# Performance work log

Measured on AMD Instinct MI355X. Metric: run time of the kernel, lower is better.

Reference implementation:

```python
import jax, jax.numpy as jnp
import numpy as np

NUM_HEADS = 16
ROPE_BASE = 2048.0


def _rope_tables(seq_len, head_dim, dtype):
    inv_freq = 1.0 / (ROPE_BASE ** (jnp.arange(0, head_dim, 2, dtype=jnp.float32) / head_dim))
    t = jnp.arange(seq_len, dtype=jnp.float32)
    freqs = jnp.einsum('i,j->ij', t, inv_freq)          # [N, D/2]
    emb = jnp.concatenate([freqs, freqs], axis=-1)       # [N, D]
    return jnp.cos(emb).astype(dtype), jnp.sin(emb).astype(dtype)


def _rotate_half(x):
    x1, x2 = jnp.split(x, 2, axis=-1)
    return jnp.concatenate([-x2, x1], axis=-1)


def setup_inputs() -> dict:
    key = jax.random.key(0)
    k1, k2, k3, k4 = jax.random.split(key, 4)
    B, N, C = 2, 2048, 1024
    x = jax.random.normal(k1, (B, N, C), dtype=jnp.float32)
    w_qkv = jax.random.normal(k2, (3 * C, C), dtype=jnp.float32) * (C ** -0.5)
    w_proj = jax.random.normal(k3, (C, C), dtype=jnp.float32) * (C ** -0.5)
    b_proj = jnp.zeros((C,), dtype=jnp.float32)
    key_padding_mask = jax.random.randint(k4, (B, N), 0, 2, dtype=jnp.int32)
    return {"x": x, "w_qkv": w_qkv, "w_proj": w_proj, "b_proj": b_proj,
            "key_padding_mask": key_padding_mask}


def reference(x, w_qkv, w_proj, b_proj, key_padding_mask):
    B, N, C = x.shape
    H = NUM_HEADS
    D = C // H
    scale = D ** -0.5

    qkv = x @ w_qkv.T                                    # [B, N, 3C]
    q, k, v = jnp.split(qkv, 3, axis=-1)
    # [B, N, C] -> [B, H, N, D]
    q = q.reshape(B, N, H, D).transpose(0, 2, 1, 3)
    k = k.reshape(B, N, H, D).transpose(0, 2, 1, 3)
    v = v.reshape(B, N, H, D).transpose(0, 2, 1, 3)

    cos, sin = _rope_tables(N, D, x.dtype)               # [N, D]
    q = q * cos + _rotate_half(q) * sin
    k = k * cos + _rotate_half(k) * sin

    attn = jnp.einsum('bhqd,bhkd->bhqk', q, k) * scale   # [B, H, N, N]
    mask = (key_padding_mask == 0)[:, None, None, :]     # [B, 1, 1, N]
    attn = jnp.where(mask, jnp.asarray(-1e9, attn.dtype), attn)
    attn = jax.nn.softmax(attn, axis=-1)

    out = jnp.einsum('bhqk,bhkd->bhqd', attn, v)         # [B, H, N, D]
    out = out.transpose(0, 2, 1, 3).reshape(B, N, C)
    return out @ w_proj.T + b_proj
```

## Files before the change

### kernel.cpp

```cpp
#include <hip/hip_runtime.h>


typedef __attribute__((ext_vector_type(8))) short          s16x8;
typedef __attribute__((ext_vector_type(8))) unsigned short u16x8;
typedef __attribute__((ext_vector_type(4))) unsigned short u16x4;
typedef __attribute__((ext_vector_type(4))) float          f32x4;
typedef __attribute__((ext_vector_type(16))) float         f32x16;
typedef __attribute__((ext_vector_type(4))) unsigned int   u32x4;

#define MFMA_BF16(a, b, c) __builtin_amdgcn_mfma_f32_16x16x32_bf16((a), (b), (c), 0, 0, 0)
#define MFMA32_BF16(a, b, c) __builtin_amdgcn_mfma_f32_32x32x16_bf16((a), (b), (c), 0, 0, 0)

#define GLD_TO_LDS(gp, lp) __builtin_amdgcn_global_load_lds(                  \
    (const __attribute__((address_space(1))) void*)(gp),                      \
    (__attribute__((address_space(3))) void*)(lp), 16, 0, 0)

__device__ __forceinline__ unsigned short f2bf(float f) {
    union { float f; unsigned int u; } v; v.f = f;
    unsigned int u = v.u;
    unsigned int r = u + 0x7FFFu + ((u >> 16) & 1u);
    return (unsigned short)(r >> 16);
}
__device__ __forceinline__ float bf2f(unsigned short h) {
    union { unsigned int u; float f; } v; v.u = ((unsigned int)h) << 16;
    return v.f;
}
__device__ __forceinline__ f32x16 zero16() {
    f32x16 z;
#pragma unroll
    for (int i = 0; i < 16; i++) z[i] = 0.f;
    return z;
}
__device__ __forceinline__ unsigned int pkbf(float a, float b) {
    return __builtin_amdgcn_perm(__builtin_bit_cast(unsigned int, b),
                                 __builtin_bit_cast(unsigned int, a), 0x07060302u);
}
__device__ __forceinline__ int perm16(int p) {
    return (p & 3) + 8 * ((p >> 2) & 1) + 4 * (p >> 3);
}

__global__ __launch_bounds__(256) void prep(const float* __restrict__ x,
                                            const float* __restrict__ wqkv,
                                            const float* __restrict__ wproj,
                                            const int* __restrict__ m,
                                            unsigned short* __restrict__ xb,
                                            unsigned short* __restrict__ wqkvb,
                                            unsigned short* __restrict__ wprojb,
                                            unsigned short* __restrict__ mb) {
    int blk = blockIdx.x, tid = threadIdx.x;
    if (blk < 4096) {
        const float* src; unsigned short* dst; int i;
        if (blk < 2048)      { src = x;     dst = xb;     i = blk * 256 + tid; }
        else if (blk < 3584) { src = wqkv;  dst = wqkvb;  i = (blk - 2048) * 256 + tid; }
        else                 { src = wproj; dst = wprojb; i = (blk - 3584) * 256 + tid; }
        f32x4 v0 = ((const f32x4*)src)[i * 2];
        f32x4 v1 = ((const f32x4*)src)[i * 2 + 1];
        u16x8 o;
        o[0] = f2bf(v0[0]); o[1] = f2bf(v0[1]); o[2] = f2bf(v0[2]); o[3] = f2bf(v0[3]);
        o[4] = f2bf(v1[0]); o[5] = f2bf(v1[1]); o[6] = f2bf(v1[2]); o[7] = f2bf(v1[3]);
        ((u16x8*)dst)[i] = o;
    } else {
        int i = (blk - 4096) * 256 + tid;
        int src = (i & ~15) | perm16(i & 15);
        mb[i] = (m[src] == 0) ? (unsigned short)0 : (unsigned short)0x3F80;
    }
}

__global__ __launch_bounds__(256) void gemm_bt(const unsigned short* __restrict__ A,
                                               const unsigned short* __restrict__ B,
                                               unsigned short* __restrict__ C,
                                               int M, int N, int K) {
    __shared__ unsigned short Al[128][64];
    __shared__ unsigned short Bl[128][64];
    const int tid  = threadIdx.x;
    const int lane = tid & 63;
    const int qd   = lane >> 4;
    const int cc   = lane & 15;
    const int wave = tid >> 6;
    const int wr   = wave >> 1, wc = wave & 1;
    const int nbx  = N >> 7;
    const int nwg  = gridDim.x;
    int d = blockIdx.x;
    int s = (nwg % 8 == 0) ? (d % 8) * (nwg / 8) + d / 8 : d;
    const int m0   = (s / nbx) * 128, n0 = (s % nbx) * 128;
    unsigned short* Alf = &Al[0][0];
    unsigned short* Blf = &Bl[0][0];

    f32x4 acc[4][4];
#pragma unroll
    for (int i = 0; i < 4; i++)
#pragma unroll
        for (int j = 0; j < 4; j++) acc[i][j] = (f32x4){0.f, 0.f, 0.f, 0.f};

    for (int k0 = 0; k0 < K; k0 += 64) {
#pragma unroll
        for (int t = 0; t < 4; t++) {
            int idx = t * 256 + tid;
            int row = idx >> 3, sg = (idx & 7) ^ (row & 7);
            GLD_TO_LDS(A + (size_t)(m0 + row) * K + k0 + sg * 8, Alf + idx * 8);
            GLD_TO_LDS(B + (size_t)(n0 + row) * K + k0 + sg * 8, Blf + idx * 8);
        }
        __syncthreads();
#pragma unroll
        for (int ks = 0; ks < 64; ks += 32) {
            const int s4 = ks >> 3;
            s16x8 af[4], bf[4];
#pragma unroll
            for (int i = 0; i < 4; i++) {
                int r = wr * 64 + i * 16 + cc;
                af[i] = *(const s16x8*)&Al[r][((s4 + qd) ^ (r & 7)) * 8];
            }
#pragma unroll
            for (int j = 0; j < 4; j++) {
                int r = wc * 64 + j * 16 + cc;
                bf[j] = *(const s16x8*)&Bl[r][((s4 + qd) ^ (r & 7)) * 8];
            }
#pragma unroll
            for (int i = 0; i < 4; i++)
#pragma unroll
                for (int j = 0; j < 4; j++)
                    acc[i][j] = MFMA_BF16(af[i], bf[j], acc[i][j]);
        }
        __syncthreads();
    }
#pragma unroll
    for (int i = 0; i < 4; i++)
#pragma unroll
        for (int j = 0; j < 4; j++)
#pragma unroll
            for (int r = 0; r < 4; r++) {
                int row = m0 + wr * 64 + i * 16 + qd * 4 + r;
                int col = n0 + wc * 64 + j * 16 + cc;
                C[(size_t)row * N + col] = f2bf(acc[i][j][r]);
            }
}

__global__ __launch_bounds__(256) void rope_scatter(const unsigned short* __restrict__ qkv,
                                                    const int* __restrict__ msk,
                                                    unsigned short* __restrict__ Kg,
                                                    unsigned short* __restrict__ Vt) {
    const int N = 2048, H = 16, D = 64, C3 = 3072;
    __shared__ unsigned short vl[64][65];
    const int nt = blockIdx.x, h = blockIdx.y, b = blockIdx.z;
    const int n0 = nt * 64;
    const int tid = threadIdx.x;
    const size_t bh = (size_t)b * H + h;
#pragma unroll
    for (int it = 0; it < 2; it++) {
        int idx = tid + it * 256;
        int row = idx >> 3, seg = idx & 7;
        int d0 = seg * 8;
        int n = n0 + row;
        size_t rb = ((size_t)b * N + n) * C3;
        int keep = msk[(size_t)b * N + n];
        u16x8 kv = *(const u16x8*)&qkv[rb + 1024 + h * 64 + d0];
        u16x8 kp = *(const u16x8*)&qkv[rb + 1024 + h * 64 + (d0 ^ 32)];
        u16x8 vv = *(const u16x8*)&qkv[rb + 2048 + h * 64 + d0];
        u16x8 ko;
        float sgn = (d0 < 32) ? -1.0f : 1.0f;
#pragma unroll
        for (int j = 0; j < 8; j++) {
            int jj = (d0 & 31) + j;
            float th = (float)n * exp2f(-0.34375f * (float)jj);
            float cth = __cosf(th), sth = __sinf(th);
            ko[j] = f2bf(bf2f(kv[j]) * cth + sgn * bf2f(kp[j]) * sth);
            vl[row][d0 + j] = keep ? vv[j] : (unsigned short)0;
        }
        *(u16x8*)&Kg[(bh * N + n) * D + d0] = ko;
    }
    __syncthreads();
#pragma unroll
    for (int it = 0; it < 2; it++) {
        int idx = tid + it * 256;
        int drow = idx >> 3, nseg = idx & 7;
        u16x8 ov;
#pragma unroll
        for (int j = 0; j < 8; j++) {
            int cpos = nseg * 8 + j;
            int srcl = (cpos & ~15) | perm16(cpos & 15);
            ov[j] = vl[srcl][drow];
        }
        *(u16x8*)&Vt[(bh * D + drow) * N + n0 + nseg * 8] = ov;
    }
}

__global__ __launch_bounds__(256, 2) void flash_attn(const unsigned short* __restrict__ qkvp,
                                                     const unsigned short* __restrict__ Kg,
                                                     const unsigned short* __restrict__ Vt,
                                                     const unsigned short* __restrict__ mb,
                                                     unsigned short* __restrict__ Og) {
    const int N = 2048, H = 16, D = 64;
    const float SCL = 0.18033688f;
    __shared__ unsigned short ldsbuf[4 * 64 * 64];
    unsigned short (*Kl0)[64] = (unsigned short(*)[64])(ldsbuf);
    unsigned short (*Kl1)[64] = (unsigned short(*)[64])(ldsbuf + 4096);
    unsigned short (*Vl0)[64] = (unsigned short(*)[64])(ldsbuf + 8192);
    unsigned short (*Vl1)[64] = (unsigned short(*)[64])(ldsbuf + 12288);
    const int tid  = threadIdx.x;
    const int lane = tid & 63;
    const int wave = tid >> 6;
    const int qhalf = wave & 1;
    const int khalf = wave >> 1;
    const int c    = lane & 31;
    const int hi   = lane >> 5;
    int dd = blockIdx.x;
    int sw = (dd & 7) * 64 + (dd >> 3);
    const int qt = sw & 15, h = (sw >> 4) & 15, b = sw >> 8;
    const int q0 = qt * 128;
    const size_t bh = (size_t)b * H + h;

    s16x8 qf[2][4];
    {
        s16x8 qraw[2][4];
#pragma unroll
        for (int qs = 0; qs < 2; qs++) {
            const unsigned short* Qb =
                qkvp + ((size_t)b * N + q0 + qhalf * 64 + qs * 32 + c) * 3072 + h * 64;
#pragma unroll
            for (int kd = 0; kd < 4; kd++)
                qraw[qs][kd] = *(const s16x8*)(Qb + kd * 16 + hi * 8);
        }
#pragma unroll
        for (int qs = 0; qs < 2; qs++) {
            float nn = (float)(q0 + qhalf * 64 + qs * 32 + c);
#pragma unroll
            for (int kd = 0; kd < 4; kd++) {
                float sgn = (kd < 2) ? -1.0f : 1.0f;
#pragma unroll
                for (int j = 0; j < 8; j++) {
                    int jj = (kd & 1) * 16 + hi * 8 + j;
                    float th = nn * exp2f(-0.34375f * (float)jj);
                    float cth = __cosf(th), sth = __sinf(th);
                    float v = bf2f((unsigned short)qraw[qs][kd][j]);
                    float p = bf2f((unsigned short)qraw[qs][kd ^ 2][j]);
                    qf[qs][kd][j] = (short)f2bf((v * cth + sgn * p * sth) * SCL);
                }
            }
        }
    }

    f32x16 o[2][2], lacc[2];
#pragma unroll
    for (int qs = 0; qs < 2; qs++) {
        o[qs][0] = zero16(); o[qs][1] = zero16(); lacc[qs] = zero16();
    }

    const unsigned short* Kbase = Kg + bh * N * D;
    const unsigned short* Vbase = Vt + bh * D * N;
    const unsigned short* mbase = mb + (size_t)b * N;
    const int row_s = tid >> 3, sg_s = (tid & 7) ^ ((tid >> 3) & 7);
    const int row_s2 = (tid + 256) >> 3, sg_s2 = (tid & 7) ^ (((tid + 256) >> 3) & 7);

    auto issue = [&](int k0, unsigned short* Kb, unsigned short* Vb) {
        GLD_TO_LDS(Kbase + (size_t)(k0 + row_s) * D + sg_s * 8,   Kb + tid * 8);
        GLD_TO_LDS(Vbase + (size_t)row_s * N + k0 + sg_s * 8,     Vb + tid * 8);
        GLD_TO_LDS(Kbase + (size_t)(k0 + row_s2) * D + sg_s2 * 8, Kb + (tid + 256) * 8);
        GLD_TO_LDS(Vbase + (size_t)row_s2 * N + k0 + sg_s2 * 8,   Vb + (tid + 256) * 8);
    };

    auto compute = [&](int k0, const unsigned short (*Kb)[64], const unsigned short (*Vb)[64]) {
        auto packkg = [&](const f32x16& sstv, s16x8* pa) {
            float p[16];
#pragma unroll
            for (int r = 0; r < 16; r++) p[r] = __builtin_amdgcn_exp2f(sstv[r]);
#pragma unroll
            for (int half = 0; half < 2; half++) {
                int bs = half * 8;
                u32x4 w = { pkbf(p[bs + 0], p[bs + 1]), pkbf(p[bs + 2], p[bs + 3]),
                            pkbf(p[bs + 4], p[bs + 5]), pkbf(p[bs + 6], p[bs + 7]) };
                pa[half] = __builtin_bit_cast(s16x8, w);
            }
        };

        int kr = khalf * 32 + c;
        s16x8 kf[4];
#pragma unroll
        for (int kd = 0; kd < 4; kd++)
            kf[kd] = *(const s16x8*)&Kb[kr][((kd * 2 + hi) ^ (kr & 7)) * 8];
        f32x16 sst0 = zero16(), sst1 = zero16();
        __builtin_amdgcn_s_setprio(1);
#pragma unroll
        for (int kd = 0; kd < 4; kd++) {
            sst0 = MFMA32_BF16(kf[kd], qf[0][kd], sst0);
            sst1 = MFMA32_BF16(kf[kd], qf[1][kd], sst1);
        }
        __builtin_amdgcn_s_setprio(0);
        s16x8 pa[2][2];
        packkg(sst0, pa[0]);
        packkg(sst1, pa[1]);

#pragma unroll
        for (int ksl = 0; ksl < 2; ksl++) {
            int ks = khalf * 2 + ksl;
            s16x8 mfr = *(const s16x8*)&mbase[k0 + ks * 16 + hi * 8];
            int vr0 = c, vr1 = 32 + c;
            s16x8 vf0 = *(const s16x8*)&Vb[vr0][((ks * 2 + hi) ^ (vr0 & 7)) * 8];
            s16x8 vf1 = *(const s16x8*)&Vb[vr1][((ks * 2 + hi) ^ (vr1 & 7)) * 8];
            __builtin_amdgcn_s_setprio(1);
#pragma unroll
            for (int qs = 0; qs < 2; qs++) {
                lacc[qs]  = MFMA32_BF16(pa[qs][ksl], mfr, lacc[qs]);
                o[qs][0]  = MFMA32_BF16(pa[qs][ksl], vf0, o[qs][0]);
                o[qs][1]  = MFMA32_BF16(pa[qs][ksl], vf1, o[qs][1]);
            }
            __builtin_amdgcn_s_setprio(0);
        }
    };

    issue(0, &Kl0[0][0], &Vl0[0][0]);
    __syncthreads();
    for (int it = 0; it < 32; it += 2) {
        int k0 = it * 64;
        if (it + 1 < 32) issue(k0 + 64, &Kl1[0][0], &Vl1[0][0]);
        compute(k0, Kl0, Vl0);
        __syncthreads();
        if (it + 2 < 32) issue(k0 + 128, &Kl0[0][0], &Vl0[0][0]);
        compute(k0 + 64, Kl1, Vl1);
        __syncthreads();
    }

    float* red = (float*)ldsbuf;
#pragma unroll
    for (int qs = 0; qs < 2; qs++) {
        __syncthreads();
        if (khalf == 1) {
            float* dst = red + qhalf * 3136 + lane * 49;
#pragma unroll
            for (int r = 0; r < 16; r++) {
                dst[r] = o[qs][0][r]; dst[16 + r] = o[qs][1][r]; dst[32 + r] = lacc[qs][r];
            }
        }
        __syncthreads();
        if (khalf == 0) {
            const float* src = red + qhalf * 3136 + lane * 49;
#pragma unroll
            for (int r = 0; r < 16; r++) {
                o[qs][0][r] += src[r]; o[qs][1][r] += src[16 + r]; lacc[qs][r] += src[32 + r];
            }
        }
    }

    if (khalf == 0) {
#pragma unroll
        for (int qs = 0; qs < 2; qs++) {
            float linv[16];
#pragma unroll
            for (int r = 0; r < 16; r++) linv[r] = 1.0f / lacc[qs][r];
#pragma unroll
            for (int db = 0; db < 2; db++)
#pragma unroll
                for (int r = 0; r < 16; r++) {
                    int n = q0 + qhalf * 64 + qs * 32 + (r & 3) + 8 * (r >> 2) + 4 * hi;
                    Og[((size_t)b * N + n) * 1024 + h * 64 + db * 32 + c] =
                        f2bf(o[qs][db][r] * linv[r]);
                }
        }
    }
}

__global__ __launch_bounds__(256) void gemm_proj(const unsigned short* __restrict__ A,
                                                 const unsigned short* __restrict__ B,
                                                 float* __restrict__ C,
                                                 const float* __restrict__ bias) {
    const int NN = 1024, K = 1024;
    __shared__ unsigned short Al[128][64];
    __shared__ unsigned short Bl[64][64];
    const int tid  = threadIdx.x;
    const int lane = tid & 63;
    const int qd   = lane >> 4;
    const int cc   = lane & 15;
    const int wave = tid >> 6;
    const int wr   = wave >> 1, wc = wave & 1;
    int dd = blockIdx.x;
    int sw = (dd & 7) * 64 + (dd >> 3);
    const int m0   = (sw >> 4) * 128, n0 = (sw & 15) * 64;
    unsigned short* Alf = &Al[0][0];
    unsigned short* Blf = &Bl[0][0];

    f32x4 acc[4][2];
#pragma unroll
    for (int i = 0; i < 4; i++)
#pragma unroll
        for (int j = 0; j < 2; j++) acc[i][j] = (f32x4){0.f, 0.f, 0.f, 0.f};

    for (int k0 = 0; k0 < K; k0 += 64) {
#pragma unroll
        for (int t = 0; t < 4; t++) {
            int idx = t * 256 + tid;
            int row = idx >> 3, sg = (idx & 7) ^ (row & 7);
            GLD_TO_LDS(A + (size_t)(m0 + row) * K + k0 + sg * 8, Alf + idx * 8);
        }
#pragma unroll
        for (int t = 0; t < 2; t++) {
            int idx = t * 256 + tid;
            int row = idx >> 3, sg = (idx & 7) ^ (row & 7);
            GLD_TO_LDS(B + (size_t)(n0 + row) * K + k0 + sg * 8, Blf + idx * 8);
        }
        __syncthreads();
#pragma unroll
        for (int ks = 0; ks < 64; ks += 32) {
            const int s4 = ks >> 3;
            s16x8 af[4], bf[2];
#pragma unroll
            for (int i = 0; i < 4; i++) {
                int r = wr * 64 + i * 16 + cc;
                af[i] = *(const s16x8*)&Al[r][((s4 + qd) ^ (r & 7)) * 8];
            }
#pragma unroll
            for (int j = 0; j < 2; j++) {
                int r = wc * 32 + j * 16 + cc;
                bf[j] = *(const s16x8*)&Bl[r][((s4 + qd) ^ (r & 7)) * 8];
            }
#pragma unroll
            for (int i = 0; i < 4; i++)
#pragma unroll
                for (int j = 0; j < 2; j++)
                    acc[i][j] = MFMA_BF16(af[i], bf[j], acc[i][j]);
        }
        __syncthreads();
    }
#pragma unroll
    for (int i = 0; i < 4; i++)
#pragma unroll
        for (int j = 0; j < 2; j++)
#pragma unroll
            for (int r = 0; r < 4; r++) {
                int row = m0 + wr * 64 + i * 16 + qd * 4 + r;
                int col = n0 + wc * 32 + j * 16 + cc;
                C[(size_t)row * NN + col] = acc[i][j][r] + bias[col];
            }
}

extern "C" void kernel_launch(void* const* d_in, const int* in_sizes, int n_in,
                              void* d_out, int out_size, void* d_ws, size_t ws_size,
                              hipStream_t stream) {
    const float* x      = (const float*)d_in[0];
    const float* w_qkv  = (const float*)d_in[1];
    const float* w_proj = (const float*)d_in[2];
    const float* b_proj = (const float*)d_in[3];
    const int*   mask   = (const int*)d_in[4];
    float* out = (float*)d_out;

    unsigned short* ws     = (unsigned short*)d_ws;
    unsigned short* xb     = ws;
    unsigned short* wqkvb  = xb     + (size_t)4096 * 1024;
    unsigned short* wprojb = wqkvb  + (size_t)3072 * 1024;
    unsigned short* qkv    = wprojb + (size_t)1024 * 1024;
    unsigned short* Qm     = qkv    + (size_t)4096 * 3072;
    unsigned short* Km     = Qm     + (size_t)32 * 2048 * 64;
    unsigned short* Vtm    = Km     + (size_t)32 * 2048 * 64;
    unsigned short* attno  = Vtm    + (size_t)32 * 2048 * 64;
    unsigned short* maskbf = attno  + (size_t)4096 * 1024;

    prep<<<4112, 256, 0, stream>>>(x, w_qkv, w_proj, mask, xb, wqkvb, wprojb, maskbf);
    gemm_bt<<<768, 256, 0, stream>>>(xb, wqkvb, qkv, 4096, 3072, 1024);
    rope_scatter<<<dim3(32, 16, 2), 256, 0, stream>>>(qkv, mask, Km, Vtm);
    flash_attn<<<512, 256, 0, stream>>>(qkv, Km, Vtm, maskbf, attno);
    gemm_proj<<<512, 256, 0, stream>>>(attno, wprojb, out, b_proj);
}
```

Measured before the change: 183.6 us.

## Fuse K RoPE into QKV GEMM epilogue and slim scatter kernel to V only

The QKV GEMM epilogue now applies the rotary embedding to the K columns and writes K straight into the head-major Km layout, because each wave's 64-column tile covers one full head, so the rotate-half partners sit in its own accumulators (j^2). The separate scatter kernel now only transposes and masks V, which removes a read of K from the qkv buffer and an extra K write-back. In exchange the GEMM epilogue does transcendental work and issues scattered 2-byte stores for the K tiles.

```diff
diff --git a/kernel.cpp b/kernel.cpp
--- a/kernel.cpp
+++ b/kernel.cpp
@@ -69,6 +69,7 @@
 __global__ __launch_bounds__(256) void gemm_bt(const unsigned short* __restrict__ A,
                                                const unsigned short* __restrict__ B,
                                                unsigned short* __restrict__ C,
+                                               unsigned short* __restrict__ Km,
                                                int M, int N, int K) {
     __shared__ unsigned short Al[128][64];
     __shared__ unsigned short Bl[128][64];
@@ -123,22 +124,46 @@
         }
         __syncthreads();
     }
-#pragma unroll
-    for (int i = 0; i < 4; i++)
-#pragma unroll
-        for (int j = 0; j < 4; j++)
+    if (n0 >= 1024 && n0 < 2048) {
+#pragma unroll
+        for (int i = 0; i < 4; i++)
 #pragma unroll
             for (int r = 0; r < 4; r++) {
                 int row = m0 + wr * 64 + i * 16 + qd * 4 + r;
-                int col = n0 + wc * 64 + j * 16 + cc;
-                C[(size_t)row * N + col] = f2bf(acc[i][j][r]);
-            }
-}
-
-__global__ __launch_bounds__(256) void rope_scatter(const unsigned short* __restrict__ qkv,
-                                                    const int* __restrict__ msk,
-                                                    unsigned short* __restrict__ Kg,
-                                                    unsigned short* __restrict__ Vt) {
+                int bb = row >> 11, n = row & 2047;
+                float cth[2], sth[2];
+#pragma unroll
+                for (int p2 = 0; p2 < 2; p2++) {
+                    float th = (float)n * exp2f(-0.34375f * (float)(p2 * 16 + cc));
+                    cth[p2] = __cosf(th); sth[p2] = __sinf(th);
+                }
+#pragma unroll
+                for (int j = 0; j < 4; j++) {
+                    int kcol = n0 - 1024 + wc * 64 + j * 16 + cc;
+                    int h = kcol >> 6, dd2 = kcol & 63;
+                    float sgn = (j < 2) ? -1.0f : 1.0f;
+                    float v = acc[i][j][r], p = acc[i][j ^ 2][r];
+                    Km[((size_t)(bb * 16 + h) * 2048 + n) * 64 + dd2] =
+                        f2bf(v * cth[j & 1] + sgn * p * sth[j & 1]);
+                }
+            }
+    } else {
+#pragma unroll
+        for (int i = 0; i < 4; i++)
+#pragma unroll
+            for (int j = 0; j < 4; j++)
+#pragma unroll
+                for (int r = 0; r < 4; r++) {
+                    int row = m0 + wr * 64 + i * 16 + qd * 4 + r;
+                    int col = n0 + wc * 64 + j * 16 + cc;
+                    C[(size_t)row * N + col] = f2bf(acc[i][j][r]);
+                }
+    }
+}
+
+__global__ __launch_bounds__(256) void v_scatter(const unsigned short* __restrict__ qkv,
+                                                 const int* __restrict__ msk,
+                                                 unsigned short* __restrict__ Vt) {
     const int N = 2048, H = 16, D = 64, C3 = 3072;
     __shared__ unsigned short vl[64][65];
     const int nt = blockIdx.x, h = blockIdx.y, b = blockIdx.z;
@@ -151,22 +176,10 @@
         int row = idx >> 3, seg = idx & 7;
         int d0 = seg * 8;
         int n = n0 + row;
-        size_t rb = ((size_t)b * N + n) * C3;
         int keep = msk[(size_t)b * N + n];
-        u16x8 kv = *(const u16x8*)&qkv[rb + 1024 + h * 64 + d0];
-        u16x8 kp = *(const u16x8*)&qkv[rb + 1024 + h * 64 + (d0 ^ 32)];
-        u16x8 vv = *(const u16x8*)&qkv[rb + 2048 + h * 64 + d0];
-        u16x8 ko;
-        float sgn = (d0 < 32) ? -1.0f : 1.0f;
-#pragma unroll
-        for (int j = 0; j < 8; j++) {
-            int jj = (d0 & 31) + j;
-            float th = (float)n * exp2f(-0.34375f * (float)jj);
-            float cth = __cosf(th), sth = __sinf(th);
-            ko[j] = f2bf(bf2f(kv[j]) * cth + sgn * bf2f(kp[j]) * sth);
-            vl[row][d0 + j] = keep ? vv[j] : (unsigned short)0;
-        }
-        *(u16x8*)&Kg[(bh * N + n) * D + d0] = ko;
+        u16x8 vv = *(const u16x8*)&qkv[((size_t)b * N + n) * C3 + 2048 + h * 64 + d0];
+#pragma unroll
+        for (int j = 0; j < 8; j++) vl[row][d0 + j] = keep ? vv[j] : (unsigned short)0;
     }
     __syncthreads();
 #pragma unroll
@@ -453,8 +466,8 @@
     unsigned short* maskbf = attno  + (size_t)4096 * 1024;
 
     prep<<<4112, 256, 0, stream>>>(x, w_qkv, w_proj, mask, xb, wqkvb, wprojb, maskbf);
-    gemm_bt<<<768, 256, 0, stream>>>(xb, wqkvb, qkv, 4096, 3072, 1024);
-    rope_scatter<<<dim3(32, 16, 2), 256, 0, stream>>>(qkv, mask, Km, Vtm);
+    gemm_bt<<<768, 256, 0, stream>>>(xb, wqkvb, qkv, Km, 4096, 3072, 1024);
+    v_scatter<<<dim3(32, 16, 2), 256, 0, stream>>>(qkv, mask, Vtm);
     flash_attn<<<512, 256, 0, stream>>>(qkv, Km, Vtm, maskbf, attno);
     gemm_proj<<<512, 256, 0, stream>>>(attno, wprojb, out, b_proj);
 }
```

Result: faster. 179.1 us (-2.4%).
